# Optimization experiments

Hardware: AMD Instinct MI355X
Metric: run time of the kernel (lower is better)

The kernel has to match this reference:

```python
import jax, jax.numpy as jnp
import numpy as np

H = 8          # num heads
DK = 64        # d_model // H
D_MODEL = 512
WIN = 256


def setup_inputs() -> dict:
    key = jax.random.key(0)
    ks = jax.random.split(key, 12)
    B, S = 2, 2048
    mk = lambda k, shape, s=1.0: jax.random.normal(k, shape, dtype=jnp.float32) * s
    inp = {
        "query": mk(ks[0], (B, S, D_MODEL)),
        "key_in": mk(ks[1], (B, S, D_MODEL)),
        "value": mk(ks[2], (B, S, D_MODEL)),
        # nn.Linear(d_model, d_model) weights (out,in) and biases, x4
        "Wq": mk(ks[3], (D_MODEL, D_MODEL), 0.02), "bq": jnp.zeros((D_MODEL,), jnp.float32),
        "Wk": mk(ks[4], (D_MODEL, D_MODEL), 0.02), "bk": jnp.zeros((D_MODEL,), jnp.float32),
        "Wv": mk(ks[5], (D_MODEL, D_MODEL), 0.02), "bv": jnp.zeros((D_MODEL,), jnp.float32),
        "Wo": mk(ks[6], (D_MODEL, D_MODEL), 0.02), "bo": jnp.zeros((D_MODEL,), jnp.float32),
    }
    return inp


def reference(query, key_in, value, Wq, bq, Wk, bk, Wv, bv, Wo, bo):
    B, S, D = query.shape
    scale = np.float32(1.0 / np.sqrt(DK))

    def proj(x, W, b):
        # (B,S,D) -> (B,H,S,DK)
        return (x @ W.T + b).reshape(B, S, H, DK).transpose(0, 2, 1, 3)

    q = proj(query, Wq, bq)
    k = proj(key_in, Wk, bk)
    v = proj(value, Wv, bv)

    # Faithful to naive_masked_matmul: full (B,H,S,S) scores, with entries
    # OUTSIDE the sliding window left at exactly 0.0 (NOT -inf) before softmax.
    scores = jnp.einsum('bhid,bhjd->bhij', q, k) * scale
    idx = jnp.arange(S)
    band = jnp.abs(idx[:, None] - idx[None, :]) <= (WIN // 2)  # (S,S) bool
    scores = jnp.where(band, scores, jnp.float32(0.0))

    p_attn = jax.nn.softmax(scores, axis=-1)
    x = jnp.einsum('bhij,bhjd->bhid', p_attn, v)          # (B,H,S,DK)
    x = x.transpose(0, 2, 1, 3).reshape(B, S, D)          # (B,S,D)
    return x @ Wo.T + bo
```

## Files before the change

kernel.cpp:

```cpp
#include <hip/hip_runtime.h>
#include <hip/hip_bf16.h>

#define SS 2048
#define DD 512
#define HWIN 128

typedef __bf16 bf16x8 __attribute__((ext_vector_type(8)));
typedef unsigned short u16x8 __attribute__((ext_vector_type(8)));
typedef float f32x4 __attribute__((ext_vector_type(4)));

__device__ __forceinline__ unsigned short f2bf(float x) {
    unsigned u = __builtin_bit_cast(unsigned, x);
    return (unsigned short)((u + 0x7fffu + ((u >> 16) & 1u)) >> 16);
}
__device__ __forceinline__ float bf2f(unsigned short s) {
    unsigned u = ((unsigned)s) << 16;
    return __builtin_bit_cast(float, u);
}
__device__ __forceinline__ void split_bf(float x, unsigned short& h, unsigned short& l) {
    h = f2bf(x);
    l = f2bf(x - bf2f(h));
}
__device__ __forceinline__ f32x4 mfma16(u16x8 a, u16x8 b, f32x4 c) {
    return __builtin_amdgcn_mfma_f32_16x16x32_bf16(
        __builtin_bit_cast(bf16x8, a), __builtin_bit_cast(bf16x8, b), c, 0, 0, 0);
}
__device__ __forceinline__ void gload16(const unsigned short* g, unsigned short* l) {
    __builtin_amdgcn_global_load_lds(
        (const __attribute__((address_space(1))) unsigned int*)g,
        (__attribute__((address_space(3))) unsigned int*)l, 16, 0, 0);
}

__global__ __launch_bounds__(256) void castAll(
    const float* __restrict__ q, const float* __restrict__ k, const float* __restrict__ v,
    const float* __restrict__ wq, const float* __restrict__ wk,
    const float* __restrict__ wv, const float* __restrict__ wo,
    unsigned short* __restrict__ QAh, unsigned short* __restrict__ KAh,
    unsigned short* __restrict__ VAh,
    unsigned short* __restrict__ WQh, unsigned short* __restrict__ WKh,
    unsigned short* __restrict__ WVh, unsigned short* __restrict__ WoP,
    float* __restrict__ VS)
{
    if (blockIdx.x == 0) {
        float4 zz = {0.f, 0.f, 0.f, 0.f};
        *(float4*)(VS + threadIdx.x * 4) = zz;
    }
    const size_t e0 = ((size_t)blockIdx.x * 256 + threadIdx.x) * 8;
    const float* src; size_t off; unsigned short* dsth; bool paired = false;
    if      (e0 < 2097152) { src = q; off = e0;           dsth = QAh + off; }
    else if (e0 < 4194304) { src = k; off = e0 - 2097152; dsth = KAh + off; }
    else if (e0 < 6291456) { src = v; off = e0 - 4194304; dsth = VAh + off; }
    else {
        const size_t e = e0 - 6291456;
        if      (e < 262144) { src = wq; off = e;          dsth = WQh + off; }
        else if (e < 524288) { src = wk; off = e - 262144; dsth = WKh + off; }
        else if (e < 786432) { src = wv; off = e - 524288; dsth = WVh + off; }
        else { src = wo; off = e - 786432; dsth = WoP + 2 * (e - 786432); paired = true; }
    }
    const float4 f0 = *(const float4*)(src + off), f1 = *(const float4*)(src + off + 4);
    const float vals[8] = {f0.x, f0.y, f0.z, f0.w, f1.x, f1.y, f1.z, f1.w};
    u16x8 h;
    #pragma unroll
    for (int i = 0; i < 8; ++i) h[i] = f2bf(vals[i]);
    *(u16x8*)dsth = h;
    if (paired) {
        u16x8 l;
        #pragma unroll
        for (int i = 0; i < 8; ++i) l[i] = f2bf(vals[i] - bf2f(h[i]));
        *(u16x8*)(dsth + 8) = l;
    }
}

__global__ __launch_bounds__(256) void proj_gemm(
    const unsigned short* __restrict__ QAh, const unsigned short* __restrict__ KAh,
    const unsigned short* __restrict__ VAh,
    const unsigned short* __restrict__ WQh, const unsigned short* __restrict__ WKh,
    const unsigned short* __restrict__ WVh,
    const float* __restrict__ bq, const float* __restrict__ bk, const float* __restrict__ bv,
    unsigned short* __restrict__ base,
    unsigned short* __restrict__ VTH, float* __restrict__ VS)
{
    const int d = blockIdx.x;
    const int hi = d >> 6, low = d & 63;
    const int x = low >> 3, rsw = low & 7;
    const int g = hi * 8 + rsw;
    const int y = g / 3, z = g - y * 3;

    const unsigned short* Ap = (z == 0) ? QAh : ((z == 1) ? KAh : VAh);
    const unsigned short* Wp = (z == 0) ? WQh : ((z == 1) ? WKh : WVh);
    const float* bias = (z == 0) ? bq : ((z == 1) ? bk : bv);
    unsigned short* OH = base + (size_t)z * 4194304;

    const int m0 = y * 128, n0 = x * 64;

    __shared__ unsigned short Ah[8 * 64 * 8];
    __shared__ unsigned short Bh[4 * 64 * 8];

    const int tid = threadIdx.x, wave = tid >> 6, lane = tid & 63;
    const int lm = lane & 15, lq = lane >> 4;
    const int wm = wave >> 1, wn = wave & 1;
    const int kb = lq * 8;

    f32x4 acc[4][2] = {};

    const int ar0 = m0 + (wave * 2 + 0) * 16 + lm;
    const int ar1 = m0 + (wave * 2 + 1) * 16 + lm;
    const int br  = n0 + wave * 16 + lm;

    const int aoff0 = ((wave * 2 + 0) * 64 + lane) * 8;
    const int aoff1 = ((wave * 2 + 1) * 64 + lane) * 8;
    const int boff  = (wave * 64 + lane) * 8;

    for (int k0 = 0; k0 < 512; k0 += 32) {
        __syncthreads();
        gload16(Ap + (size_t)ar0 * 512 + k0 + kb, &Ah[aoff0]);
        gload16(Ap + (size_t)ar1 * 512 + k0 + kb, &Ah[aoff1]);
        gload16(Wp + (size_t)br  * 512 + k0 + kb, &Bh[boff]);
        __syncthreads();

        u16x8 afh[4], bfh[2];
        #pragma unroll
        for (int i = 0; i < 4; ++i)
            afh[i] = *(const u16x8*)&Ah[((wm * 4 + i) * 64 + lane) * 8];
        #pragma unroll
        for (int j = 0; j < 2; ++j)
            bfh[j] = *(const u16x8*)&Bh[((wn * 2 + j) * 64 + lane) * 8];
        #pragma unroll
        for (int i = 0; i < 4; ++i)
            #pragma unroll
            for (int j = 0; j < 2; ++j)
                acc[i][j] = mfma16(afh[i], bfh[j], acc[i][j]);
    }

    if (z < 2) {
        #pragma unroll
        for (int i = 0; i < 4; ++i)
            #pragma unroll
            for (int j = 0; j < 2; ++j) {
                const int col = n0 + (wn * 2 + j) * 16 + lm;
                const float bv_ = bias[col];
                #pragma unroll
                for (int r = 0; r < 4; ++r) {
                    const int row = m0 + (wm * 4 + i) * 16 + lq * 4 + r;
                    OH[(size_t)row * 512 + col] = f2bf(acc[i][j][r] + bv_);
                }
            }
    } else {
        float csum[2] = {0.f, 0.f};
        #pragma unroll
        for (int i = 0; i < 4; ++i)
            #pragma unroll
            for (int j = 0; j < 2; ++j) {
                const int col = n0 + (wn * 2 + j) * 16 + lm;
                const float bv_ = bias[col];
                #pragma unroll
                for (int r = 0; r < 4; ++r) {
                    const int row = m0 + (wm * 4 + i) * 16 + lq * 4 + r;
                    const float vv = acc[i][j][r] + bv_;
                    csum[j] += vv;
                    const size_t vix =
                        (((size_t)(row >> 11) * 8 + (col >> 6)) * 64 + (col & 63)) * 2048
                        + (row & 2047);
                    VTH[vix] = f2bf(vv);
                }
            }
        #pragma unroll
        for (int j = 0; j < 2; ++j) {
            float s = csum[j];
            s += __shfl_xor(s, 16);
            s += __shfl_xor(s, 32);
            if (lq == 0) {
                const int col = n0 + (wn * 2 + j) * 16 + lm;
                atomicAdd(&VS[(m0 >> 11) * 512 + col], s);
            }
        }
    }
}

__global__ __launch_bounds__(256) void out_gemm(
    const unsigned short* __restrict__ XHg, const unsigned short* __restrict__ XLg,
    const unsigned short* __restrict__ WoP, const float* __restrict__ bo,
    float* __restrict__ O)
{
    const int gid = blockIdx.x;
    const int rr = gid & 7, hi = gid >> 3;
    const int nblk = hi & 7, mhi = hi >> 3;
    const int mblk = mhi * 8 + rr;
    const int m0 = mblk * 64, n0 = nblk * 64;

    __shared__ unsigned short Ah[2 * 4096], Al[2 * 4096];
    __shared__ unsigned short Bh[2 * 4096], Bl[2 * 4096];

    const int tid = threadIdx.x, wave = tid >> 6, lane = tid & 63;
    const int lm = lane & 15, lq = lane >> 4;
    const int kb = lq * 8;

    f32x4 acc[4] = {};

    const int arow = m0 + wave * 16 + lm;
    const int brow = n0 + wave * 16 + lm;

    #define OSTAGE(k0_, bs)                                                     \
    {                                                                           \
        _Pragma("unroll")                                                       \
        for (int s = 0; s < 2; ++s) {                                           \
            const int o = (bs) * 4096 + ((s * 4 + wave) * 64 + lane) * 8;       \
            gload16(XHg + (size_t)arow * 512 + (k0_) + s * 32 + kb, &Ah[o]);    \
            gload16(XLg + (size_t)arow * 512 + (k0_) + s * 32 + kb, &Al[o]);    \
            const unsigned short* pw =                                          \
                WoP + 2 * ((size_t)brow * 512 + (k0_) + s * 32 + kb);           \
            gload16(pw,     &Bh[o]);                                            \
            gload16(pw + 8, &Bl[o]);                                            \
        }                                                                       \
    }

    OSTAGE(0, 0);
    __syncthreads();

    for (int t = 0; t < 8; ++t) {
        const int cur = t & 1;
        if (t < 7) OSTAGE((t + 1) * 64, cur ^ 1);

        #pragma unroll
        for (int s = 0; s < 2; ++s) {
            const u16x8 a_h = *(const u16x8*)&Ah[cur * 4096 + ((s * 4 + wave) * 64 + lane) * 8];
            const u16x8 a_l = *(const u16x8*)&Al[cur * 4096 + ((s * 4 + wave) * 64 + lane) * 8];
            #pragma unroll
            for (int j = 0; j < 4; ++j) {
                const u16x8 b_h = *(const u16x8*)&Bh[cur * 4096 + ((s * 4 + j) * 64 + lane) * 8];
                const u16x8 b_l = *(const u16x8*)&Bl[cur * 4096 + ((s * 4 + j) * 64 + lane) * 8];
                acc[j] = mfma16(a_h, b_h, acc[j]);
                acc[j] = mfma16(a_h, b_l, acc[j]);
                acc[j] = mfma16(a_l, b_h, acc[j]);
            }
        }

        __syncthreads();
    }
    #undef OSTAGE

    #pragma unroll
    for (int j = 0; j < 4; ++j) {
        const int col = n0 + j * 16 + lm;
        const float bv_ = bo[col];
        #pragma unroll
        for (int r = 0; r < 4; ++r) {
            const int row = m0 + wave * 16 + lq * 4 + r;
            O[(size_t)row * 512 + col] = acc[j][r] + bv_;
        }
    }
}

__global__ __launch_bounds__(256) void attn_mfma(
    const unsigned short* __restrict__ QH, const unsigned short* __restrict__ KH,
    const unsigned short* __restrict__ VTH, const float* __restrict__ VS,
    unsigned short* __restrict__ XH, unsigned short* __restrict__ XL)
{
    const int dblk = blockIdx.x;
    const int bhi = dblk >> 8, blow = dblk & 255;
    const int xblk = blow >> 3, rrs = blow & 7;
    const int bh = bhi * 8 + rrs;
    const int h = bh & 7, b = bh >> 3;
    const int i0 = xblk * 64;
    const int tid = threadIdx.x, wave = tid >> 6, lane = tid & 63;
    const int lm = lane & 15, lq = lane >> 4;
    const int kb = lq * 8;

    __shared__ unsigned short KfH[2 * 8 * 64 * 8];
    __shared__ unsigned short VfH[2 * 8 * 64 * 8];
    __shared__ unsigned short Swh[64][72];

    const size_t qoff = ((size_t)(b * SS + i0 + wave * 16 + lm)) * DD + h * 64 + kb;
    const u16x8 aQ0h = *(const u16x8*)(QH + qoff);
    const u16x8 aQ1h = *(const u16x8*)(QH + qoff + 32);

    f32x4 oacc[4] = {};
    float dacc[4] = {0.f, 0.f, 0.f, 0.f};

    const size_t vrow = ((size_t)bh * 64 + wave * 16 + lm) * 2048;
    const int s0 = (wave * 2 + 0) * 64 * 8 + lane * 8;
    const int s1 = (wave * 2 + 1) * 64 * 8 + lane * 8;

    #define STAGE(jt_, bufsel)                                                  \
    {                                                                           \
        const int jt0_ = i0 - 128 + (jt_) * 64;                                 \
        const int jrow = jt0_ + wave * 16 + lm;                                 \
        const int jrc = min(max(jrow, 0), SS - 1);                              \
        const size_t kgb = ((size_t)(b * SS + jrc)) * DD + h * 64 + kb;         \
        gload16(KH + kgb,      &KfH[(bufsel) * 4096 + s0]);                     \
        gload16(KH + kgb + 32, &KfH[(bufsel) * 4096 + s1]);                     \
        const int j0c = min(max(jt0_ + kb, 0), SS - 8);                         \
        const int j1c = min(max(jt0_ + 32 + kb, 0), SS - 8);                    \
        gload16(VTH + vrow + j0c, &VfH[(bufsel) * 4096 + s0]);                  \
        gload16(VTH + vrow + j1c, &VfH[(bufsel) * 4096 + s1]);                  \
    }

    STAGE(0, 0);
    __syncthreads();

    for (int jt = 0; jt < 5; ++jt) {
        const int buf = jt & 1;
        if (jt < 4) STAGE(jt + 1, buf ^ 1);
        const int jt0 = i0 - 128 + jt * 64;
        const int rmin = i0 + wave * 16;

        #pragma unroll
        for (int js = 0; js < 4; ++js) {
            const int j0 = js * 16;
            const int cmin = jt0 + j0, cmax = cmin + 15;
            const bool skip = (cmax < 0) || (cmin >= SS) ||
                              (cmax < rmin - HWIN) || (cmin > rmin + 15 + HWIN);
            if (skip) {
                #pragma unroll
                for (int r = 0; r < 4; ++r)
                    Swh[wave * 16 + lq * 4 + r][j0 + lm] = 0;
                continue;
            }
            const u16x8 bK0h = *(const u16x8*)&KfH[buf * 4096 + ((js * 2 + 0) * 64 + lane) * 8];
            const u16x8 bK1h = *(const u16x8*)&KfH[buf * 4096 + ((js * 2 + 1) * 64 + lane) * 8];
            f32x4 s = {0.f, 0.f, 0.f, 0.f};
            s = mfma16(aQ0h, bK0h, s);
            s = mfma16(aQ1h, bK1h, s);
            const int jg = jt0 + j0 + lm;
            const int iq = i0 + wave * 16 + lq * 4;
            #pragma unroll
            for (int r = 0; r < 4; ++r) {
                const int qi = iq + r;
                const bool in = (jg >= 0) && (jg < SS) &&
                                (jg >= qi - HWIN) && (jg <= qi + HWIN);
                const float w = in ? (__expf(s[r] * 0.125f) - 1.0f) : 0.0f;
                dacc[r] += w;
                Swh[wave * 16 + lq * 4 + r][j0 + lm] = f2bf(w);
            }
        }

        const u16x8 aP0h = *(const u16x8*)&Swh[wave * 16 + lm][kb];
        const u16x8 aP1h = *(const u16x8*)&Swh[wave * 16 + lm][kb + 32];
        #pragma unroll
        for (int s4 = 0; s4 < 4; ++s4) {
            const u16x8 bV0h = *(const u16x8*)&VfH[buf * 4096 + ((s4 * 2 + 0) * 64 + lane) * 8];
            const u16x8 bV1h = *(const u16x8*)&VfH[buf * 4096 + ((s4 * 2 + 1) * 64 + lane) * 8];
            oacc[s4] = mfma16(aP0h, bV0h, oacc[s4]);
            oacc[s4] = mfma16(aP1h, bV1h, oacc[s4]);
        }
        __syncthreads();
    }
    #undef STAGE

    #pragma unroll
    for (int r = 0; r < 4; ++r) {
        float v = dacc[r];
        v += __shfl_xor(v, 1);
        v += __shfl_xor(v, 2);
        v += __shfl_xor(v, 4);
        v += __shfl_xor(v, 8);
        dacc[r] = v + 2048.0f;
    }

    #pragma unroll
    for (int s4 = 0; s4 < 4; ++s4) {
        const float vsv = VS[bh * 64 + s4 * 16 + lm];
        #pragma unroll
        for (int r = 0; r < 4; ++r) {
            const int qrow = i0 + wave * 16 + lq * 4 + r;
            const float x = (oacc[s4][r] + vsv) / dacc[r];
            unsigned short xh, xl;
            split_bf(x, xh, xl);
            const size_t ix = ((size_t)(b * SS + qrow)) * DD + h * 64 + s4 * 16 + lm;
            XH[ix] = xh;
            XL[ix] = xl;
        }
    }
}

extern "C" void kernel_launch(void* const* d_in, const int* in_sizes, int n_in,
                              void* d_out, int out_size, void* d_ws, size_t ws_size,
                              hipStream_t stream)
{
    const float* query  = (const float*)d_in[0];
    const float* key_in = (const float*)d_in[1];
    const float* value  = (const float*)d_in[2];
    const float* Wq = (const float*)d_in[3]; const float* bq = (const float*)d_in[4];
    const float* Wk = (const float*)d_in[5]; const float* bk = (const float*)d_in[6];
    const float* Wv = (const float*)d_in[7]; const float* bv = (const float*)d_in[8];
    const float* Wo = (const float*)d_in[9]; const float* bo = (const float*)d_in[10];

    unsigned short* wsb = (unsigned short*)d_ws;
    unsigned short* QH  = wsb;
    unsigned short* KH  = wsb + 4194304;
    unsigned short* VTH = wsb + 8388608;
    unsigned short* XH  = wsb + 12582912;
    unsigned short* XL  = wsb + 14680064;
    unsigned short* WQh = wsb + 16777216;
    unsigned short* WKh = wsb + 17039360;
    unsigned short* WVh = wsb + 17301504;
    unsigned short* WoP = wsb + 17825792;
    unsigned short* QAh = wsb + 18350080;
    unsigned short* KAh = wsb + 20447232;
    unsigned short* VAh = wsb + 22544384;
    float* VSp  = (float*)((char*)d_ws + 63045632);

    castAll<<<3584, 256, 0, stream>>>(query, key_in, value, Wq, Wk, Wv, Wo,
                                      QAh, KAh, VAh, WQh, WKh, WVh, WoP, VSp);

    proj_gemm<<<768, 256, 0, stream>>>(QAh, KAh, VAh, WQh, WKh, WVh,
                                       bq, bk, bv, QH, VTH, VSp);

    attn_mfma<<<512, 256, 0, stream>>>(QH, KH, VTH, VSp, XH, XL);

    out_gemm<<<512, 256, 0, stream>>>(XH, XL, WoP, bo, (float*)d_out);
}
```

Measured before the change: 146.4 us.

## Fuse fp32-to-bf16 input casts into projection GEMM and drop atomics for V sums

Removes the separate cast pass over the activations and Q/K/V weights. The projection GEMM now loads fp32 directly, converts to bf16 in registers and stores to LDS, which cuts the intermediate bf16 write and read-back. The V column-sum atomics and their zero-init are replaced by per-tile partial sums that attention reduces with 32 loads each. In exchange the projection GEMM reads twice the bytes per tile through plain synchronous loads instead of async global-to-LDS loads, and the loads are not overlapped with compute.

Result: slower. 160.2 us (+9.5%).

```diff
diff --git a/kernel.cpp b/kernel.cpp
--- a/kernel.cpp
+++ b/kernel.cpp
@@ -20,6 +20,13 @@
 __device__ __forceinline__ void split_bf(float x, unsigned short& h, unsigned short& l) {
     h = f2bf(x);
     l = f2bf(x - bf2f(h));
+}
+__device__ __forceinline__ u16x8 cvt8(float4 f0, float4 f1) {
+    const float vals[8] = {f0.x, f0.y, f0.z, f0.w, f1.x, f1.y, f1.z, f1.w};
+    u16x8 h;
+    #pragma unroll
+    for (int i = 0; i < 8; ++i) h[i] = f2bf(vals[i]);
+    return h;
 }
 __device__ __forceinline__ f32x4 mfma16(u16x8 a, u16x8 b, f32x4 c) {
     return __builtin_amdgcn_mfma_f32_16x16x32_bf16(
@@ -31,54 +38,29 @@
         (__attribute__((address_space(3))) unsigned int*)l, 16, 0, 0);
 }
 
-__global__ __launch_bounds__(256) void castAll(
+__global__ __launch_bounds__(256) void castWo(
+    const float* __restrict__ wo, unsigned short* __restrict__ WoP)
+{
+    const size_t e0 = ((size_t)blockIdx.x * 256 + threadIdx.x) * 8;
+    const float4 f0 = *(const float4*)(wo + e0), f1 = *(const float4*)(wo + e0 + 4);
+    const float vals[8] = {f0.x, f0.y, f0.z, f0.w, f1.x, f1.y, f1.z, f1.w};
+    u16x8 h, l;
+    #pragma unroll
+    for (int i = 0; i < 8; ++i) {
+        unsigned short hh, ll;
+        split_bf(vals[i], hh, ll);
+        h[i] = hh; l[i] = ll;
+    }
+    *(u16x8*)(WoP + 2 * e0)     = h;
+    *(u16x8*)(WoP + 2 * e0 + 8) = l;
+}
+
+__global__ __launch_bounds__(256) void proj_gemm(
     const float* __restrict__ q, const float* __restrict__ k, const float* __restrict__ v,
-    const float* __restrict__ wq, const float* __restrict__ wk,
-    const float* __restrict__ wv, const float* __restrict__ wo,
-    unsigned short* __restrict__ QAh, unsigned short* __restrict__ KAh,
-    unsigned short* __restrict__ VAh,
-    unsigned short* __restrict__ WQh, unsigned short* __restrict__ WKh,
-    unsigned short* __restrict__ WVh, unsigned short* __restrict__ WoP,
-    float* __restrict__ VS)
-{
-    if (blockIdx.x == 0) {
-        float4 zz = {0.f, 0.f, 0.f, 0.f};
-        *(float4*)(VS + threadIdx.x * 4) = zz;
-    }
-    const size_t e0 = ((size_t)blockIdx.x * 256 + threadIdx.x) * 8;
-    const float* src; size_t off; unsigned short* dsth; bool paired = false;
-    if      (e0 < 2097152) { src = q; off = e0;           dsth = QAh + off; }
-    else if (e0 < 4194304) { src = k; off = e0 - 2097152; dsth = KAh + off; }
-    else if (e0 < 6291456) { src = v; off = e0 - 4194304; dsth = VAh + off; }
-    else {
-        const size_t e = e0 - 6291456;
-        if      (e < 262144) { src = wq; off = e;          dsth = WQh + off; }
-        else if (e < 524288) { src = wk; off = e - 262144; dsth = WKh + off; }
-        else if (e < 786432) { src = wv; off = e - 524288; dsth = WVh + off; }
-        else { src = wo; off = e - 786432; dsth = WoP + 2 * (e - 786432); paired = true; }
-    }
-    const float4 f0 = *(const float4*)(src + off), f1 = *(const float4*)(src + off + 4);
-    const float vals[8] = {f0.x, f0.y, f0.z, f0.w, f1.x, f1.y, f1.z, f1.w};
-    u16x8 h;
-    #pragma unroll
-    for (int i = 0; i < 8; ++i) h[i] = f2bf(vals[i]);
-    *(u16x8*)dsth = h;
-    if (paired) {
-        u16x8 l;
-        #pragma unroll
-        for (int i = 0; i < 8; ++i) l[i] = f2bf(vals[i] - bf2f(h[i]));
-        *(u16x8*)(dsth + 8) = l;
-    }
-}
-
-__global__ __launch_bounds__(256) void proj_gemm(
-    const unsigned short* __restrict__ QAh, const unsigned short* __restrict__ KAh,
-    const unsigned short* __restrict__ VAh,
-    const unsigned short* __restrict__ WQh, const unsigned short* __restrict__ WKh,
-    const unsigned short* __restrict__ WVh,
+    const float* __restrict__ wq, const float* __restrict__ wk, const float* __restrict__ wv,
     const float* __restrict__ bq, const float* __restrict__ bk, const float* __restrict__ bv,
     unsigned short* __restrict__ base,
-    unsigned short* __restrict__ VTH, float* __restrict__ VS)
+    unsigned short* __restrict__ VTH, float* __restrict__ part)
 {
     const int d = blockIdx.x;
     const int hi = d >> 6, low = d & 63;
@@ -86,8 +68,8 @@
     const int g = hi * 8 + rsw;
     const int y = g / 3, z = g - y * 3;
 
-    const unsigned short* Ap = (z == 0) ? QAh : ((z == 1) ? KAh : VAh);
-    const unsigned short* Wp = (z == 0) ? WQh : ((z == 1) ? WKh : WVh);
+    const float* Ap = (z == 0) ? q : ((z == 1) ? k : v);
+    const float* Wp = (z == 0) ? wq : ((z == 1) ? wk : wv);
     const float* bias = (z == 0) ? bq : ((z == 1) ? bk : bv);
     unsigned short* OH = base + (size_t)z * 4194304;
 
@@ -112,10 +94,17 @@
     const int boff  = (wave * 64 + lane) * 8;
 
     for (int k0 = 0; k0 < 512; k0 += 32) {
+        const float* pa0 = Ap + (size_t)ar0 * 512 + k0 + kb;
+        const float* pa1 = Ap + (size_t)ar1 * 512 + k0 + kb;
+        const float* pw  = Wp + (size_t)br  * 512 + k0 + kb;
+        const float4 a00 = *(const float4*)pa0, a01 = *(const float4*)(pa0 + 4);
+        const float4 a10 = *(const float4*)pa1, a11 = *(const float4*)(pa1 + 4);
+        const float4 w0  = *(const float4*)pw,  w1  = *(const float4*)(pw + 4);
+
         __syncthreads();
-        gload16(Ap + (size_t)ar0 * 512 + k0 + kb, &Ah[aoff0]);
-        gload16(Ap + (size_t)ar1 * 512 + k0 + kb, &Ah[aoff1]);
-        gload16(Wp + (size_t)br  * 512 + k0 + kb, &Bh[boff]);
+        *(u16x8*)&Ah[aoff0] = cvt8(a00, a01);
+        *(u16x8*)&Ah[aoff1] = cvt8(a10, a11);
+        *(u16x8*)&Bh[boff]  = cvt8(w0, w1);
         __syncthreads();
 
         u16x8 afh[4], bfh[2];
@@ -171,7 +160,7 @@
             s += __shfl_xor(s, 32);
             if (lq == 0) {
                 const int col = n0 + (wn * 2 + j) * 16 + lm;
-                atomicAdd(&VS[(m0 >> 11) * 512 + col], s);
+                part[(size_t)(y * 2 + wm) * 512 + col] = s;
             }
         }
     }
@@ -253,7 +242,7 @@
 
 __global__ __launch_bounds__(256) void attn_mfma(
     const unsigned short* __restrict__ QH, const unsigned short* __restrict__ KH,
-    const unsigned short* __restrict__ VTH, const float* __restrict__ VS,
+    const unsigned short* __restrict__ VTH, const float* __restrict__ part,
     unsigned short* __restrict__ XH, unsigned short* __restrict__ XL)
 {
     const int dblk = blockIdx.x;
@@ -359,7 +348,10 @@
 
     #pragma unroll
     for (int s4 = 0; s4 < 4; ++s4) {
-        const float vsv = VS[bh * 64 + s4 * 16 + lm];
+        const float* pp = part + (size_t)(b * 32) * 512 + h * 64 + s4 * 16 + lm;
+        float vsv = 0.f;
+        #pragma unroll 8
+        for (int p = 0; p < 32; ++p) vsv += pp[(size_t)p * 512];
         #pragma unroll
         for (int r = 0; r < 4; ++r) {
             const int qrow = i0 + wave * 16 + lq * 4 + r;
@@ -391,22 +383,15 @@
     unsigned short* VTH = wsb + 8388608;
     unsigned short* XH  = wsb + 12582912;
     unsigned short* XL  = wsb + 14680064;
-    unsigned short* WQh = wsb + 16777216;
-    unsigned short* WKh = wsb + 17039360;
-    unsigned short* WVh = wsb + 17301504;
-    unsigned short* WoP = wsb + 17825792;
-    unsigned short* QAh = wsb + 18350080;
-    unsigned short* KAh = wsb + 20447232;
-    unsigned short* VAh = wsb + 22544384;
-    float* VSp  = (float*)((char*)d_ws + 63045632);
-
-    castAll<<<3584, 256, 0, stream>>>(query, key_in, value, Wq, Wk, Wv, Wo,
-                                      QAh, KAh, VAh, WQh, WKh, WVh, WoP, VSp);
-
-    proj_gemm<<<768, 256, 0, stream>>>(QAh, KAh, VAh, WQh, WKh, WVh,
-                                       bq, bk, bv, QH, VTH, VSp);
-
-    attn_mfma<<<512, 256, 0, stream>>>(QH, KH, VTH, VSp, XH, XL);
+    unsigned short* WoP = wsb + 16777216;
+    float* partp = (float*)((char*)d_ws + 63045632);
+
+    castWo<<<128, 256, 0, stream>>>(Wo, WoP);
+
+    proj_gemm<<<768, 256, 0, stream>>>(query, key_in, value, Wq, Wk, Wv,
+                                       bq, bk, bv, QH, VTH, partp);
+
+    attn_mfma<<<512, 256, 0, stream>>>(QH, KH, VTH, partp, XH, XL);
 
     out_gemm<<<512, 256, 0, stream>>>(XH, XL, WoP, bo, (float*)d_out);
 }
```
